# Performance work log

Measured on AMD Instinct MI355X. Metric: run time of the kernel, lower is better.

The kernel has to match this reference:

```python
import jax, jax.numpy as jnp
import numpy as np

FEATS = 1024
HEAD = 16
DH = FEATS // HEAD
B, N = 2, 2048
SQRT_D = FEATS ** 0.5  # note: source scales by sqrt(feats), not sqrt(head_dim)


def setup_inputs() -> dict:
    key = jax.random.key(0)
    ks = jax.random.split(key, 9)
    s = 1.0 / np.sqrt(FEATS)
    return {
        "x": jax.random.normal(ks[0], (B, N, FEATS), dtype=jnp.float32),
        "Wq": jax.random.normal(ks[1], (FEATS, FEATS), dtype=jnp.float32) * s,
        "bq": jax.random.normal(ks[2], (FEATS,), dtype=jnp.float32) * s,
        "Wk": jax.random.normal(ks[3], (FEATS, FEATS), dtype=jnp.float32) * s,
        "bk": jax.random.normal(ks[4], (FEATS,), dtype=jnp.float32) * s,
        "Wv": jax.random.normal(ks[5], (FEATS, FEATS), dtype=jnp.float32) * s,
        "bv": jax.random.normal(ks[6], (FEATS,), dtype=jnp.float32) * s,
        "Wo": jax.random.normal(ks[7], (FEATS, FEATS), dtype=jnp.float32) * s,
        "bo": jax.random.normal(ks[8], (FEATS,), dtype=jnp.float32) * s,
    }


def reference(x, Wq, bq, Wk, bk, Wv, bv, Wo, bo):
    b, n, f = x.shape
    # Linear layers: y = x @ W^T + b (torch nn.Linear convention)
    q = (x @ Wq.T + bq).reshape(b, n, HEAD, DH).transpose(0, 2, 1, 3)  # bhnd
    k = (x @ Wk.T + bk).reshape(b, n, HEAD, DH).transpose(0, 2, 1, 3)
    v = (x @ Wv.T + bv).reshape(b, n, HEAD, DH).transpose(0, 2, 1, 3)
    score = jax.nn.softmax(jnp.einsum('bhif,bhjf->bhij', q, k) / SQRT_D, axis=-1)
    attn = jnp.einsum('bhij,bhjf->bihf', score, v)  # [b, n, head, dh]
    o = attn.reshape(b, n, f) @ Wo.T + bo
    return o
```

## Files before the change

### kernel.cpp

```cpp
#include <hip/hip_runtime.h>
#include <stdint.h>

typedef short short8 __attribute__((ext_vector_type(8)));
typedef float f32x4 __attribute__((ext_vector_type(4)));
typedef float f32x16 __attribute__((ext_vector_type(16)));
typedef unsigned int uint2v __attribute__((ext_vector_type(2)));
typedef unsigned int uint4v __attribute__((ext_vector_type(4)));

#define SEQ 2048
#define NBH 32

__device__ __forceinline__ unsigned short f32_to_bf16(float f) {
  union { float f; uint32_t u; } v; v.f = f;
  return (unsigned short)((v.u + 0x7fffu + ((v.u >> 16) & 1u)) >> 16);
}

__device__ __forceinline__ float bf16_to_f32(unsigned short u) {
  union { uint32_t u; float f; } v; v.u = ((uint32_t)u) << 16;
  return v.f;
}

__device__ __forceinline__ unsigned int cvtpk_bf16(float lo, float hi) {
  unsigned int r;
  asm("v_cvt_pk_bf16_f32 %0, %1, %2" : "=v"(r) : "v"(lo), "v"(hi));
  return r;
}

__device__ __forceinline__ void gload_lds16(const unsigned short* g, unsigned short* l) {
  __builtin_amdgcn_global_load_lds(
      (const __attribute__((address_space(1))) unsigned int*)g,
      (__attribute__((address_space(3))) unsigned int*)l, 16, 0, 0);
}

__global__ void cast_f32_bf16(const float* __restrict__ in,
                              unsigned short* __restrict__ out, int n4) {
  int i = blockIdx.x * blockDim.x + threadIdx.x;
  if (i >= n4) return;
  float4 v = ((const float4*)in)[i];
  ushort4 o;
  o.x = f32_to_bf16(v.x); o.y = f32_to_bf16(v.y);
  o.z = f32_to_bf16(v.z); o.w = f32_to_bf16(v.w);
  ((ushort4*)out)[i] = o;
}

#define GSWZ(row, k) ((k) ^ ((row) & 3) ^ (((row) >> 2) & 3))

__device__ __forceinline__ void gemm_core_1024(
    const unsigned short* __restrict__ Ag,
    const unsigned short* __restrict__ Bg,
    int tid, f32x4 acc[4][4])
{
  __shared__ __align__(16) unsigned short As[128 * 32];
  __shared__ __align__(16) unsigned short Bs[128 * 32];
  const int w = tid >> 6, l = tid & 63;
  const int wr = w >> 1, wc = w & 1;
  const int lc = l & 15, lg = l >> 4;

  const int c0row = tid >> 2,        c0ks = tid & 3;
  const int c1row = (256 + tid) >> 2;

  for (int k0 = 0; k0 < 1024; k0 += 32) {
    int kg0 = GSWZ(c0row, c0ks);
    int kg1 = GSWZ(c1row, c0ks);
    gload_lds16(Ag + (size_t)c0row * 1024 + k0 + kg0 * 8, As + (w * 64) * 8);
    gload_lds16(Ag + (size_t)c1row * 1024 + k0 + kg1 * 8, As + (256 + w * 64) * 8);
    gload_lds16(Bg + (size_t)c0row * 1024 + k0 + kg0 * 8, Bs + (w * 64) * 8);
    gload_lds16(Bg + (size_t)c1row * 1024 + k0 + kg1 * 8, Bs + (256 + w * 64) * 8);
    __syncthreads();

    short8 a[4], b[4];
#pragma unroll
    for (int mi = 0; mi < 4; ++mi) {
      int row = wr * 64 + mi * 16 + lc;
      int ko = GSWZ(row, lg);
      a[mi] = *(const short8*)(As + row * 32 + ko * 8);
    }
#pragma unroll
    for (int ni = 0; ni < 4; ++ni) {
      int row = wc * 64 + ni * 16 + lc;
      int ko = GSWZ(row, lg);
      b[ni] = *(const short8*)(Bs + row * 32 + ko * 8);
    }
#pragma unroll
    for (int mi = 0; mi < 4; ++mi)
#pragma unroll
      for (int ni = 0; ni < 4; ++ni)
        acc[mi][ni] = __builtin_amdgcn_mfma_f32_16x16x32_bf16(a[mi], b[ni], acc[mi][ni], 0, 0, 0);
    __syncthreads();
  }
}

__global__ __launch_bounds__(256, 2)
void gemm_qkv(const unsigned short* __restrict__ XB,
              const unsigned short* __restrict__ WQB,
              const unsigned short* __restrict__ WKB,
              const unsigned short* __restrict__ WVB,
              const float* __restrict__ bq,
              const float* __restrict__ bk,
              const float* __restrict__ bv,
              unsigned short* __restrict__ Qo,
              unsigned short* __restrict__ Ko,
              unsigned short* __restrict__ Vo)
{
  const int tid = threadIdx.x;
  const int tm = blockIdx.x * 128;
  const int tn = blockIdx.y * 128;
  const int wi = tn >> 10;
  const int tnl = tn & 1023;
  const unsigned short* Bw = (wi == 0 ? WQB : wi == 1 ? WKB : WVB) + (size_t)tnl * 1024;
  const float* bias = (wi == 0 ? bq : wi == 1 ? bk : bv);
  unsigned short* Out = (wi == 0 ? Qo : wi == 1 ? Ko : Vo);
  const float qscale = (wi == 0) ? 0.04508422002778011f : 1.0f;

  f32x4 acc[4][4];
#pragma unroll
  for (int mi = 0; mi < 4; ++mi)
#pragma unroll
    for (int ni = 0; ni < 4; ++ni)
      acc[mi][ni] = (f32x4){0.f, 0.f, 0.f, 0.f};

  gemm_core_1024(XB + (size_t)tm * 1024, Bw, tid, acc);

  const int w = tid >> 6, l = tid & 63;
  const int wr = w >> 1, wc = w & 1;
  const int lc = l & 15, lg = l >> 4;
#pragma unroll
  for (int ni = 0; ni < 4; ++ni) {
    int nl = tnl + wc * 64 + ni * 16 + lc;
    float bb = bias[nl];
    int h = nl >> 6, d = nl & 63;
#pragma unroll
    for (int mi = 0; mi < 4; ++mi) {
#pragma unroll
      for (int r = 0; r < 4; ++r) {
        int m = tm + wr * 64 + mi * 16 + lg * 4 + r;
        int b = m >> 11, i = m & 2047;
        float v = (acc[mi][ni][r] + bb) * qscale;
        Out[(((size_t)(b * 16 + h) * SEQ + i) << 6) + d] = f32_to_bf16(v);
      }
    }
  }
}

__global__ __launch_bounds__(256, 2)
void gemm_o(const unsigned short* __restrict__ AT,
            const unsigned short* __restrict__ WOB,
            const float* __restrict__ bo,
            float* __restrict__ Of)
{
  const int tid = threadIdx.x;
  const int tm = blockIdx.x * 128;
  const int tn = blockIdx.y * 128;

  f32x4 acc[4][4];
#pragma unroll
  for (int mi = 0; mi < 4; ++mi)
#pragma unroll
    for (int ni = 0; ni < 4; ++ni)
      acc[mi][ni] = (f32x4){0.f, 0.f, 0.f, 0.f};

  gemm_core_1024(AT + (size_t)tm * 1024, WOB + (size_t)tn * 1024, tid, acc);

  const int w = tid >> 6, l = tid & 63;
  const int wr = w >> 1, wc = w & 1;
  const int lc = l & 15, lg = l >> 4;
#pragma unroll
  for (int ni = 0; ni < 4; ++ni) {
    int n = tn + wc * 64 + ni * 16 + lc;
    float bb = bo[n];
#pragma unroll
    for (int mi = 0; mi < 4; ++mi) {
#pragma unroll
      for (int r = 0; r < 4; ++r) {
        int m = tm + wr * 64 + mi * 16 + lg * 4 + r;
        Of[(size_t)m * 1024 + n] = acc[mi][ni][r] + bb;
      }
    }
  }
}

__global__ void transpose_v(const unsigned short* __restrict__ V,
                            unsigned short* __restrict__ VT)
{
  __shared__ unsigned short tile[32][33];
  int bh = blockIdx.z;
  int n0 = blockIdx.x * 32, d0 = blockIdx.y * 32;
  int x = threadIdx.x;
  for (int yy = threadIdx.y; yy < 32; yy += 8)
    tile[yy][x] = V[((size_t)bh * SEQ + n0 + yy) * 64 + d0 + x];
  __syncthreads();
  for (int yy = threadIdx.y; yy < 32; yy += 8)
    VT[((size_t)bh * 64 + d0 + yy) * SEQ + n0 + x] = tile[x][yy];
}

__global__ __launch_bounds__(256, 4)
void attn_fwd7(const unsigned short* __restrict__ Qm,
               const unsigned short* __restrict__ Km,
               const unsigned short* __restrict__ VTm,
               unsigned short* __restrict__ Op0,
               unsigned short* __restrict__ Op1,
               float* __restrict__ Lp)
{
  __shared__ __align__(16) unsigned short KV[2][64 * 128];
  const int tid = threadIdx.x, w = tid >> 6, l = tid & 63;
  const int lq = l & 31, hi = l >> 5;
  const int m15 = lq & 15;
  const int bh = blockIdx.x, q0 = blockIdx.y * 128;
  const int js = blockIdx.z;
  const int j0 = js << 10;

  const unsigned short* Qb = Qm + ((size_t)bh * SEQ + q0 + w * 32) * 64;
  const unsigned short* Kg = Km + ((size_t)bh * SEQ + j0) * 64;
  const unsigned short* Vg = VTm + (size_t)bh * 64 * SEQ + j0;

  const int sr = l >> 4;
  const int ss = l & 15;
  const unsigned short* sp[4];
  int sstep[4];
#pragma unroll
  for (int i = 0; i < 4; ++i) {
    int r = w * 16 + i * 4 + sr;
    int t = ss ^ (i * 4 + sr);
    if (t < 8) { sp[i] = Kg + (size_t)r * 64 + t * 8;          sstep[i] = 64 * 64; }
    else       { sp[i] = Vg + (size_t)r * SEQ + (t - 8) * 8;   sstep[i] = 64; }
  }

  short8 qf[4];
#pragma unroll
  for (int kc = 0; kc < 4; ++kc)
    qf[kc] = *(const short8*)(Qb + lq * 64 + kc * 16 + hi * 8);

  f32x16 o0, o1;
#pragma unroll
  for (int r = 0; r < 16; ++r) { o0[r] = 0.f; o1[r] = 0.f; }
  float sm[8];
#pragma unroll
  for (int i = 0; i < 8; ++i) sm[i] = 0.f;

#pragma unroll
  for (int i = 0; i < 4; ++i) {
    gload_lds16(sp[i], &KV[0][(w * 16 + i * 4) * 128]);
    sp[i] += sstep[i];
  }
  __syncthreads();

  for (int t = 0; t < 16; ++t) {
    const int cur = t & 1;
    if (t + 1 < 16) {
#pragma unroll
      for (int i = 0; i < 4; ++i) {
        gload_lds16(sp[i], &KV[cur ^ 1][(w * 16 + i * 4) * 128]);
        sp[i] += sstep[i];
      }
    }
    const char* Tb = (const char*)(&KV[cur][0]);

    f32x16 s0, s1;
#pragma unroll
    for (int r = 0; r < 16; ++r) { s0[r] = 0.f; s1[r] = 0.f; }
    __builtin_amdgcn_s_setprio(1);
#pragma unroll
    for (int kc = 0; kc < 4; ++kc) {
      short8 kf = *(const short8*)(Tb + lq * 256 + (((kc * 2 + hi) ^ m15) << 4));
      s0 = __builtin_amdgcn_mfma_f32_32x32x16_bf16(kf, qf[kc], s0, 0, 0, 0);
    }
#pragma unroll
    for (int kc = 0; kc < 4; ++kc) {
      short8 kf = *(const short8*)(Tb + (32 + lq) * 256 + (((kc * 2 + hi) ^ m15) << 4));
      s1 = __builtin_amdgcn_mfma_f32_32x32x16_bf16(kf, qf[kc], s1, 0, 0, 0);
    }
    __builtin_amdgcn_s_setprio(0);

    float p[32];
#pragma unroll
    for (int r = 0; r < 16; ++r) {
      p[r] = __builtin_amdgcn_exp2f(s0[r]);
      p[16 + r] = __builtin_amdgcn_exp2f(s1[r]);
    }
#pragma unroll
    for (int i = 0; i < 8; ++i)
      sm[i] += (p[i] + p[i + 8]) + (p[i + 16] + p[i + 24]);

    short8 pa[4];
#pragma unroll
    for (int ks = 0; ks < 4; ++ks) {
      const int pb = ks * 8;
      unsigned int a0 = cvtpk_bf16(p[pb + 0], p[pb + 1]);
      unsigned int a1 = cvtpk_bf16(p[pb + 2], p[pb + 3]);
      unsigned int b0 = cvtpk_bf16(p[pb + 4], p[pb + 5]);
      unsigned int b1 = cvtpk_bf16(p[pb + 6], p[pb + 7]);
      unsigned int a0x = __shfl_xor((int)a0, 32), b0x = __shfl_xor((int)b0, 32);
      unsigned int a1x = __shfl_xor((int)a1, 32), b1x = __shfl_xor((int)b1, 32);
      union { uint4v u; short8 s; } cvt;
      cvt.u.x = hi ? b0x : a0;
      cvt.u.y = hi ? b1x : a1;
      cvt.u.z = hi ? b0 : a0x;
      cvt.u.w = hi ? b1 : a1x;
      pa[ks] = cvt.s;
    }

    __builtin_amdgcn_s_setprio(1);
#pragma unroll
    for (int ks = 0; ks < 4; ++ks) {
      short8 vf = *(const short8*)(Tb + lq * 256 + (((8 + ks * 2 + hi) ^ m15) << 4));
      o0 = __builtin_amdgcn_mfma_f32_32x32x16_bf16(vf, pa[ks], o0, 0, 0, 0);
    }
#pragma unroll
    for (int ks = 0; ks < 4; ++ks) {
      short8 vf = *(const short8*)(Tb + (32 + lq) * 256 + (((8 + ks * 2 + hi) ^ m15) << 4));
      o1 = __builtin_amdgcn_mfma_f32_32x32x16_bf16(vf, pa[ks], o1, 0, 0, 0);
    }
    __builtin_amdgcn_s_setprio(0);
    __syncthreads();
  }

  float lden = ((sm[0] + sm[1]) + (sm[2] + sm[3])) + ((sm[4] + sm[5]) + (sm[6] + sm[7]));
  lden += __shfl_xor(lden, 32);
  const int b = bh >> 4, h = bh & 15;
  const int iq = q0 + w * 32 + lq;
  unsigned short* Op = js ? Op1 : Op0;
  if (hi == 0) Lp[(size_t)js * (NBH * SEQ) + (size_t)bh * SEQ + iq] = lden;
  const size_t obase = ((size_t)b * SEQ + iq) * 1024 + h * 64;
#pragma unroll
  for (int rq = 0; rq < 4; ++rq) {
    uint2v pk0, pk1;
    pk0.x = cvtpk_bf16(o0[rq * 4 + 0], o0[rq * 4 + 1]);
    pk0.y = cvtpk_bf16(o0[rq * 4 + 2], o0[rq * 4 + 3]);
    pk1.x = cvtpk_bf16(o1[rq * 4 + 0], o1[rq * 4 + 1]);
    pk1.y = cvtpk_bf16(o1[rq * 4 + 2], o1[rq * 4 + 3]);
    *(uint2v*)(Op + obase + rq * 8 + hi * 4) = pk0;
    *(uint2v*)(Op + obase + 32 + rq * 8 + hi * 4) = pk1;
  }
}

__global__ __launch_bounds__(256)
void attn_norm(const unsigned short* __restrict__ Op0,
               const unsigned short* __restrict__ Op1,
               const float* __restrict__ Lp,
               unsigned short* __restrict__ ATB)
{
  const int b = blockIdx.y;
  const int g = blockIdx.x * 256 + threadIdx.x;
  const size_t gi = (size_t)b * 524288 + g;
  const ushort4 a = ((const ushort4*)Op0)[gi];
  const ushort4 c = ((const ushort4*)Op1)[gi];
  const int e = g << 2;
  const int i = e >> 10, col = e & 1023, h = col >> 6;
  const size_t lix = (size_t)((b << 4) + h) * SEQ + i;
  const float inv = 1.0f / (Lp[lix] + Lp[(size_t)NBH * SEQ + lix]);
  ushort4 o;
  o.x = f32_to_bf16((bf16_to_f32(a.x) + bf16_to_f32(c.x)) * inv);
  o.y = f32_to_bf16((bf16_to_f32(a.y) + bf16_to_f32(c.y)) * inv);
  o.z = f32_to_bf16((bf16_to_f32(a.z) + bf16_to_f32(c.z)) * inv);
  o.w = f32_to_bf16((bf16_to_f32(a.w) + bf16_to_f32(c.w)) * inv);
  ((ushort4*)ATB)[gi] = o;
}

extern "C" void kernel_launch(void* const* d_in, const int* in_sizes, int n_in,
                              void* d_out, int out_size, void* d_ws, size_t ws_size,
                              hipStream_t stream) {
  (void)in_sizes; (void)n_in; (void)out_size; (void)ws_size;
  const float* x  = (const float*)d_in[0];
  const float* Wq = (const float*)d_in[1];
  const float* bq = (const float*)d_in[2];
  const float* Wk = (const float*)d_in[3];
  const float* bk = (const float*)d_in[4];
  const float* Wv = (const float*)d_in[5];
  const float* bv = (const float*)d_in[6];
  const float* Wo = (const float*)d_in[7];
  const float* bo = (const float*)d_in[8];
  float* Of = (float*)d_out;

  unsigned short* ws  = (unsigned short*)d_ws;
  unsigned short* XB  = ws;
  unsigned short* WQB = ws + 4194304u;
  unsigned short* WKB = ws + 5242880u;
  unsigned short* WVB = ws + 6291456u;
  unsigned short* WOB = ws + 7340032u;
  unsigned short* QB  = ws + 8388608u;
  unsigned short* KB  = ws + 12582912u;
  unsigned short* VB  = ws + 16777216u;
  unsigned short* VTB = ws + 20971520u;
  unsigned short* ATB = ws + 25165824u;
  unsigned short* Op0 = ws;
  unsigned short* Op1 = ws + 16777216u;
  float* Lp = (float*)(ws + 4194304u);

  cast_f32_bf16<<<4096, 256, 0, stream>>>(x,  XB,  1048576);
  cast_f32_bf16<<<1024, 256, 0, stream>>>(Wq, WQB, 262144);
  cast_f32_bf16<<<1024, 256, 0, stream>>>(Wk, WKB, 262144);
  cast_f32_bf16<<<1024, 256, 0, stream>>>(Wv, WVB, 262144);
  cast_f32_bf16<<<1024, 256, 0, stream>>>(Wo, WOB, 262144);

  gemm_qkv<<<dim3(32, 24), 256, 0, stream>>>(XB, WQB, WKB, WVB, bq, bk, bv, QB, KB, VB);
  transpose_v<<<dim3(64, 2, 32), dim3(32, 8), 0, stream>>>(VB, VTB);

  attn_fwd7<<<dim3(32, 16, 2), 256, 0, stream>>>(QB, KB, VTB, Op0, Op1, Lp);
  attn_norm<<<dim3(2048, 2), 256, 0, stream>>>(Op0, Op1, Lp, ATB);
  gemm_o<<<dim3(32, 8), 256, 0, stream>>>(ATB, WOB, bo, Of);
}
```

Before: 132.4 us.

## Fuse V transpose into QKV GEMM, software-pipeline attention, retile output GEMM

The QKV GEMM epilogue now writes V directly in transposed layout with packed bf16 stores, which removes the separate transpose kernel and its round trip through memory. The attention kernel splits K and V into separate double buffers and computes the next tile's QK^T scores while the current tile's softmax and PV run, so MFMA work overlaps with exp and shuffle work. Occupancy is lowered from 4 to 3 blocks per CU to leave room for the extra registers. The output GEMM switches to 64x128 tiles so it launches twice as many blocks, trading less data reuse per block for better CU coverage.

```diff
diff --git a/kernel.cpp b/kernel.cpp
--- a/kernel.cpp
+++ b/kernel.cpp
@@ -100,7 +100,7 @@
               const float* __restrict__ bv,
               unsigned short* __restrict__ Qo,
               unsigned short* __restrict__ Ko,
-              unsigned short* __restrict__ Vo)
+              unsigned short* __restrict__ VTo)
 {
   const int tid = threadIdx.x;
   const int tm = blockIdx.x * 128;
@@ -109,7 +109,6 @@
   const int tnl = tn & 1023;
   const unsigned short* Bw = (wi == 0 ? WQB : wi == 1 ? WKB : WVB) + (size_t)tnl * 1024;
   const float* bias = (wi == 0 ? bq : wi == 1 ? bk : bv);
-  unsigned short* Out = (wi == 0 ? Qo : wi == 1 ? Ko : Vo);
   const float qscale = (wi == 0) ? 0.04508422002778011f : 1.0f;
 
   f32x4 acc[4][4];
@@ -124,19 +123,39 @@
   const int w = tid >> 6, l = tid & 63;
   const int wr = w >> 1, wc = w & 1;
   const int lc = l & 15, lg = l >> 4;
-#pragma unroll
-  for (int ni = 0; ni < 4; ++ni) {
-    int nl = tnl + wc * 64 + ni * 16 + lc;
-    float bb = bias[nl];
-    int h = nl >> 6, d = nl & 63;
-#pragma unroll
-    for (int mi = 0; mi < 4; ++mi) {
-#pragma unroll
-      for (int r = 0; r < 4; ++r) {
-        int m = tm + wr * 64 + mi * 16 + lg * 4 + r;
-        int b = m >> 11, i = m & 2047;
-        float v = (acc[mi][ni][r] + bb) * qscale;
-        Out[(((size_t)(b * 16 + h) * SEQ + i) << 6) + d] = f32_to_bf16(v);
+
+  if (wi == 2) {
+#pragma unroll
+    for (int ni = 0; ni < 4; ++ni) {
+      int nl = tnl + wc * 64 + ni * 16 + lc;
+      float bb = bias[nl];
+      int h = nl >> 6, d = nl & 63;
+#pragma unroll
+      for (int mi = 0; mi < 4; ++mi) {
+        int ibase = tm + wr * 64 + mi * 16 + lg * 4;
+        int b = ibase >> 11, i = ibase & 2047;
+        uint2v pk;
+        pk.x = cvtpk_bf16(acc[mi][ni][0] + bb, acc[mi][ni][1] + bb);
+        pk.y = cvtpk_bf16(acc[mi][ni][2] + bb, acc[mi][ni][3] + bb);
+        *(uint2v*)(VTo + (((size_t)(b * 16 + h) * 64 + d) * SEQ + i)) = pk;
+      }
+    }
+  } else {
+    unsigned short* Out = (wi == 0) ? Qo : Ko;
+#pragma unroll
+    for (int ni = 0; ni < 4; ++ni) {
+      int nl = tnl + wc * 64 + ni * 16 + lc;
+      float bb = bias[nl];
+      int h = nl >> 6, d = nl & 63;
+#pragma unroll
+      for (int mi = 0; mi < 4; ++mi) {
+#pragma unroll
+        for (int r = 0; r < 4; ++r) {
+          int m = tm + wr * 64 + mi * 16 + lg * 4 + r;
+          int b = m >> 11, i = m & 2047;
+          float v = (acc[mi][ni][r] + bb) * qscale;
+          Out[(((size_t)(b * 16 + h) * SEQ + i) << 6) + d] = f32_to_bf16(v);
+        }
       }
     }
   }
@@ -148,60 +167,76 @@
             const float* __restrict__ bo,
             float* __restrict__ Of)
 {
+  __shared__ __align__(16) unsigned short As[64 * 32];
+  __shared__ __align__(16) unsigned short Bs[128 * 32];
   const int tid = threadIdx.x;
-  const int tm = blockIdx.x * 128;
+  const int w = tid >> 6, l = tid & 63;
+  const int lc = l & 15, lg = l >> 4;
+  const int tm = blockIdx.x * 64;
   const int tn = blockIdx.y * 128;
-
-  f32x4 acc[4][4];
+  const unsigned short* Ag = AT + (size_t)tm * 1024;
+  const unsigned short* Bg = WOB + (size_t)tn * 1024;
+
+  const int crow = tid >> 2, cks = tid & 3;
+
+  f32x4 acc[4][2];
 #pragma unroll
   for (int mi = 0; mi < 4; ++mi)
 #pragma unroll
-    for (int ni = 0; ni < 4; ++ni)
+    for (int ni = 0; ni < 2; ++ni)
       acc[mi][ni] = (f32x4){0.f, 0.f, 0.f, 0.f};
 
-  gemm_core_1024(AT + (size_t)tm * 1024, WOB + (size_t)tn * 1024, tid, acc);
-
-  const int w = tid >> 6, l = tid & 63;
-  const int wr = w >> 1, wc = w & 1;
-  const int lc = l & 15, lg = l >> 4;
-#pragma unroll
-  for (int ni = 0; ni < 4; ++ni) {
-    int n = tn + wc * 64 + ni * 16 + lc;
+  for (int k0 = 0; k0 < 1024; k0 += 32) {
+    int kg = GSWZ(crow, cks);
+    gload_lds16(Ag + (size_t)crow * 1024 + k0 + kg * 8, As + w * 512);
+    gload_lds16(Bg + (size_t)crow * 1024 + k0 + kg * 8, Bs + w * 512);
+    gload_lds16(Bg + (size_t)(64 + crow) * 1024 + k0 + kg * 8, Bs + 2048 + w * 512);
+    __syncthreads();
+
+    short8 a[4], b[2];
+#pragma unroll
+    for (int mi = 0; mi < 4; ++mi) {
+      int row = mi * 16 + lc;
+      a[mi] = *(const short8*)(As + row * 32 + GSWZ(row, lg) * 8);
+    }
+#pragma unroll
+    for (int ni = 0; ni < 2; ++ni) {
+      int row = w * 32 + ni * 16 + lc;
+      b[ni] = *(const short8*)(Bs + row * 32 + GSWZ(row, lg) * 8);
+    }
+#pragma unroll
+    for (int mi = 0; mi < 4; ++mi)
+#pragma unroll
+      for (int ni = 0; ni < 2; ++ni)
+        acc[mi][ni] = __builtin_amdgcn_mfma_f32_16x16x32_bf16(a[mi], b[ni], acc[mi][ni], 0, 0, 0);
+    __syncthreads();
+  }
+
+#pragma unroll
+  for (int ni = 0; ni < 2; ++ni) {
+    int n = tn + w * 32 + ni * 16 + lc;
     float bb = bo[n];
 #pragma unroll
     for (int mi = 0; mi < 4; ++mi) {
 #pragma unroll
       for (int r = 0; r < 4; ++r) {
-        int m = tm + wr * 64 + mi * 16 + lg * 4 + r;
+        int m = tm + mi * 16 + lg * 4 + r;
         Of[(size_t)m * 1024 + n] = acc[mi][ni][r] + bb;
       }
     }
   }
 }
 
-__global__ void transpose_v(const unsigned short* __restrict__ V,
-                            unsigned short* __restrict__ VT)
-{
-  __shared__ unsigned short tile[32][33];
-  int bh = blockIdx.z;
-  int n0 = blockIdx.x * 32, d0 = blockIdx.y * 32;
-  int x = threadIdx.x;
-  for (int yy = threadIdx.y; yy < 32; yy += 8)
-    tile[yy][x] = V[((size_t)bh * SEQ + n0 + yy) * 64 + d0 + x];
-  __syncthreads();
-  for (int yy = threadIdx.y; yy < 32; yy += 8)
-    VT[((size_t)bh * 64 + d0 + yy) * SEQ + n0 + x] = tile[x][yy];
-}
-
-__global__ __launch_bounds__(256, 4)
-void attn_fwd7(const unsigned short* __restrict__ Qm,
+__global__ __launch_bounds__(256, 3)
+void attn_fwd8(const unsigned short* __restrict__ Qm,
                const unsigned short* __restrict__ Km,
                const unsigned short* __restrict__ VTm,
                unsigned short* __restrict__ Op0,
                unsigned short* __restrict__ Op1,
                float* __restrict__ Lp)
 {
-  __shared__ __align__(16) unsigned short KV[2][64 * 128];
+  __shared__ __align__(16) unsigned short KBs[2][32 * 128];
+  __shared__ __align__(16) unsigned short VBs[2][32 * 128];
   const int tid = threadIdx.x, w = tid >> 6, l = tid & 63;
   const int lq = l & 31, hi = l >> 5;
   const int m15 = lq & 15;
@@ -213,17 +248,33 @@
   const unsigned short* Kg = Km + ((size_t)bh * SEQ + j0) * 64;
   const unsigned short* Vg = VTm + (size_t)bh * 64 * SEQ + j0;
 
-  const int sr = l >> 4;
-  const int ss = l & 15;
-  const unsigned short* sp[4];
-  int sstep[4];
-#pragma unroll
-  for (int i = 0; i < 4; ++i) {
-    int r = w * 16 + i * 4 + sr;
-    int t = ss ^ (i * 4 + sr);
-    if (t < 8) { sp[i] = Kg + (size_t)r * 64 + t * 8;          sstep[i] = 64 * 64; }
-    else       { sp[i] = Vg + (size_t)r * SEQ + (t - 8) * 8;   sstep[i] = 64; }
-  }
+  int koff[2], voff[2];
+#pragma unroll
+  for (int j = 0; j < 2; ++j) {
+    int row = w * 8 + j * 4 + (l >> 4);
+    int t = (l & 15) ^ (row & 15);
+    koff[j] = (t < 8) ? (row * 64 + t * 8) : ((32 + row) * 64 + (t - 8) * 8);
+    voff[j] = (t < 8) ? (row * SEQ + t * 8) : ((32 + row) * SEQ + (t - 8) * 8);
+  }
+
+#define STAGE_K(buf, ti) { \
+    gload_lds16(Kg + (size_t)(ti) * 4096 + koff[0], &KBs[buf][(w * 8) * 128]); \
+    gload_lds16(Kg + (size_t)(ti) * 4096 + koff[1], &KBs[buf][(w * 8 + 4) * 128]); }
+#define STAGE_V(buf, ti) { \
+    gload_lds16(Vg + (size_t)(ti) * 64 + voff[0], &VBs[buf][(w * 8) * 128]); \
+    gload_lds16(Vg + (size_t)(ti) * 64 + voff[1], &VBs[buf][(w * 8 + 4) * 128]); }
+
+#define S_COMPUTE(b, s0, s1) { \
+    const char* Kb_ = (const char*)(&KBs[b][0]); \
+    __builtin_amdgcn_s_setprio(1); \
+    _Pragma("unroll") \
+    for (int kc = 0; kc < 4; ++kc) { \
+      short8 kf0 = *(const short8*)(Kb_ + lq * 256 + (((kc * 2 + hi) ^ m15) << 4)); \
+      s0 = __builtin_amdgcn_mfma_f32_32x32x16_bf16(kf0, qf[kc], s0, 0, 0, 0); \
+      short8 kf1 = *(const short8*)(Kb_ + lq * 256 + (((8 + kc * 2 + hi) ^ m15) << 4)); \
+      s1 = __builtin_amdgcn_mfma_f32_32x32x16_bf16(kf1, qf[kc], s1, 0, 0, 0); \
+    } \
+    __builtin_amdgcn_s_setprio(0); }
 
   short8 qf[4];
 #pragma unroll
@@ -237,45 +288,30 @@
 #pragma unroll
   for (int i = 0; i < 8; ++i) sm[i] = 0.f;
 
-#pragma unroll
-  for (int i = 0; i < 4; ++i) {
-    gload_lds16(sp[i], &KV[0][(w * 16 + i * 4) * 128]);
-    sp[i] += sstep[i];
-  }
+  STAGE_K(0, 0); STAGE_V(0, 0); STAGE_K(1, 1);
   __syncthreads();
-
+  f32x16 s0p, s1p;
+#pragma unroll
+  for (int r = 0; r < 16; ++r) { s0p[r] = 0.f; s1p[r] = 0.f; }
+  S_COMPUTE(0, s0p, s1p);
+  __syncthreads();
+
+  int x = 1, y = 0;
+#pragma unroll 2
   for (int t = 0; t < 16; ++t) {
-    const int cur = t & 1;
-    if (t + 1 < 16) {
-#pragma unroll
-      for (int i = 0; i < 4; ++i) {
-        gload_lds16(sp[i], &KV[cur ^ 1][(w * 16 + i * 4) * 128]);
-        sp[i] += sstep[i];
-      }
-    }
-    const char* Tb = (const char*)(&KV[cur][0]);
-
-    f32x16 s0, s1;
-#pragma unroll
-    for (int r = 0; r < 16; ++r) { s0[r] = 0.f; s1[r] = 0.f; }
-    __builtin_amdgcn_s_setprio(1);
-#pragma unroll
-    for (int kc = 0; kc < 4; ++kc) {
-      short8 kf = *(const short8*)(Tb + lq * 256 + (((kc * 2 + hi) ^ m15) << 4));
-      s0 = __builtin_amdgcn_mfma_f32_32x32x16_bf16(kf, qf[kc], s0, 0, 0, 0);
-    }
-#pragma unroll
-    for (int kc = 0; kc < 4; ++kc) {
-      short8 kf = *(const short8*)(Tb + (32 + lq) * 256 + (((kc * 2 + hi) ^ m15) << 4));
-      s1 = __builtin_amdgcn_mfma_f32_32x32x16_bf16(kf, qf[kc], s1, 0, 0, 0);
-    }
-    __builtin_amdgcn_s_setprio(0);
+    if (t + 1 < 16) STAGE_V(y ^ 1, t + 1);
+    if (t + 2 < 16) STAGE_K(x ^ 1, t + 2);
+
+    f32x16 s0n, s1n;
+#pragma unroll
+    for (int r = 0; r < 16; ++r) { s0n[r] = 0.f; s1n[r] = 0.f; }
+    if (t + 1 < 16) S_COMPUTE(x, s0n, s1n);
 
     float p[32];
 #pragma unroll
     for (int r = 0; r < 16; ++r) {
-      p[r] = __builtin_amdgcn_exp2f(s0[r]);
-      p[16 + r] = __builtin_amdgcn_exp2f(s1[r]);
+      p[r] = __builtin_amdgcn_exp2f(s0p[r]);
+      p[16 + r] = __builtin_amdgcn_exp2f(s1p[r]);
     }
 #pragma unroll
     for (int i = 0; i < 8; ++i)
@@ -299,20 +335,25 @@
       pa[ks] = cvt.s;
     }
 
-    __builtin_amdgcn_s_setprio(1);
-#pragma unroll
-    for (int ks = 0; ks < 4; ++ks) {
-      short8 vf = *(const short8*)(Tb + lq * 256 + (((8 + ks * 2 + hi) ^ m15) << 4));
-      o0 = __builtin_amdgcn_mfma_f32_32x32x16_bf16(vf, pa[ks], o0, 0, 0, 0);
-    }
-#pragma unroll
-    for (int ks = 0; ks < 4; ++ks) {
-      short8 vf = *(const short8*)(Tb + (32 + lq) * 256 + (((8 + ks * 2 + hi) ^ m15) << 4));
-      o1 = __builtin_amdgcn_mfma_f32_32x32x16_bf16(vf, pa[ks], o1, 0, 0, 0);
-    }
-    __builtin_amdgcn_s_setprio(0);
+    {
+      const char* Vb_ = (const char*)(&VBs[y][0]);
+      __builtin_amdgcn_s_setprio(1);
+#pragma unroll
+      for (int ks = 0; ks < 4; ++ks) {
+        short8 vf0 = *(const short8*)(Vb_ + lq * 256 + (((ks * 2 + hi) ^ m15) << 4));
+        o0 = __builtin_amdgcn_mfma_f32_32x32x16_bf16(vf0, pa[ks], o0, 0, 0, 0);
+        short8 vf1 = *(const short8*)(Vb_ + lq * 256 + (((8 + ks * 2 + hi) ^ m15) << 4));
+        o1 = __builtin_amdgcn_mfma_f32_32x32x16_bf16(vf1, pa[ks], o1, 0, 0, 0);
+      }
+      __builtin_amdgcn_s_setprio(0);
+    }
     __syncthreads();
-  }
+    s0p = s0n; s1p = s1n;
+    x ^= 1; y ^= 1;
+  }
+#undef STAGE_K
+#undef STAGE_V
+#undef S_COMPUTE
 
   float lden = ((sm[0] + sm[1]) + (sm[2] + sm[3])) + ((sm[4] + sm[5]) + (sm[6] + sm[7]));
   lden += __shfl_xor(lden, 32);
@@ -379,7 +420,6 @@
   unsigned short* WOB = ws + 7340032u;
   unsigned short* QB  = ws + 8388608u;
   unsigned short* KB  = ws + 12582912u;
-  unsigned short* VB  = ws + 16777216u;
   unsigned short* VTB = ws + 20971520u;
   unsigned short* ATB = ws + 25165824u;
   unsigned short* Op0 = ws;
@@ -392,10 +432,9 @@
   cast_f32_bf16<<<1024, 256, 0, stream>>>(Wv, WVB, 262144);
   cast_f32_bf16<<<1024, 256, 0, stream>>>(Wo, WOB, 262144);
 
-  gemm_qkv<<<dim3(32, 24), 256, 0, stream>>>(XB, WQB, WKB, WVB, bq, bk, bv, QB, KB, VB);
-  transpose_v<<<dim3(64, 2, 32), dim3(32, 8), 0, stream>>>(VB, VTB);
-
-  attn_fwd7<<<dim3(32, 16, 2), 256, 0, stream>>>(QB, KB, VTB, Op0, Op1, Lp);
+  gemm_qkv<<<dim3(32, 24), 256, 0, stream>>>(XB, WQB, WKB, WVB, bq, bk, bv, QB, KB, VTB);
+
+  attn_fwd8<<<dim3(32, 16, 2), 256, 0, stream>>>(QB, KB, VTB, Op0, Op1, Lp);
   attn_norm<<<dim3(2048, 2), 256, 0, stream>>>(Op0, Op1, Lp, ATB);
-  gemm_o<<<dim3(32, 8), 256, 0, stream>>>(ATB, WOB, bo, Of);
-}
+  gemm_o<<<dim3(64, 8), 256, 0, stream>>>(ATB, WOB, bo, Of);
+}
```

After: 182.3 us. 37.7% more time.
